# Optimization experiments

Hardware: AMD Instinct MI355X
Metric: run time of the kernel (lower is better)

The kernel has to match this reference:

```python
import jax, jax.numpy as jnp
import numpy as np

L = 6          # backbone GENConv layers
N = 100000     # nodes
E = 625000     # edges
F = 128        # gnn_in_features
HID = 64       # learner hidden width
NTOT = 200000  # node-feature table rows
TASKS = 112    # num_tasks
LN_EPS = 1e-5
MSG_EPS = 1e-7


def setup_inputs() -> dict:
    key = jax.random.key(0)
    ks = iter(jax.random.split(key, 40))

    def w(shape, fan):
        return jax.random.normal(next(ks), shape, jnp.float32) / np.float32(np.sqrt(fan))

    inp = {}
    inp["x"] = jax.random.uniform(next(ks), (N, 8), jnp.float32)
    inp["node_index"] = jax.random.randint(next(ks), (N,), 0, NTOT)
    inp["edge_index"] = jax.random.randint(next(ks), (2, E), 0, N)
    inp["edge_attr"] = jax.random.normal(next(ks), (E, 8), jnp.float32)
    inp["node_features_table"] = jax.random.normal(next(ks), (NTOT, 8), jnp.float32)
    inp["W_ohe"] = w((8, 8), 8); inp["b_ohe"] = jnp.zeros((8,), jnp.float32)
    inp["W_enc"] = w((16, F), 16); inp["b_enc"] = jnp.zeros((F,), jnp.float32)
    inp["W_edge"] = w((8, F), 8); inp["b_edge"] = jnp.zeros((F,), jnp.float32)
    inp["learner_W1"] = w((L + 1, F, HID), F); inp["learner_b1"] = jnp.zeros((L + 1, HID), jnp.float32)
    inp["learner_W2"] = w((L + 1, HID, F), HID); inp["learner_b2"] = jnp.zeros((L + 1, F), jnp.float32)
    inp["gcn_W"] = w((L, F, F), F); inp["gcn_b"] = jnp.zeros((L, F), jnp.float32)
    inp["gcn_t"] = jnp.ones((L,), jnp.float32)   # learnable softmax temperature
    inp["ln_gamma"] = jnp.ones((L, F), jnp.float32); inp["ln_beta"] = jnp.zeros((L, F), jnp.float32)
    inp["W_pred"] = w((F, TASKS), F); inp["b_pred"] = jnp.zeros((TASKS,), jnp.float32)
    return inp


def _layer_norm(h, g, b):
    mu = jnp.mean(h, -1, keepdims=True)
    var = jnp.mean(jnp.square(h - mu), -1, keepdims=True)
    return g * (h - mu) * jax.lax.rsqrt(var + LN_EPS) + b


def _learner(z, W1, b1, W2, b2):
    # NodeWeightLearner: 2-layer MLP with LeakyReLU(0.2), sigmoid gate per node/feature
    z = jax.nn.leaky_relu(z @ W1 + b1, 0.2)
    return jax.nn.sigmoid(z @ W2 + b2)


def reference(x, node_index, edge_index, edge_attr, node_features_table,
              W_ohe, b_ohe, W_enc, b_enc, W_edge, b_edge,
              learner_W1, learner_b1, learner_W2, learner_b2,
              gcn_W, gcn_b, gcn_t, ln_gamma, ln_beta, W_pred, b_pred):
    src, dst = edge_index[0], edge_index[1]
    n = x.shape[0]

    nf = jnp.concatenate([node_features_table[node_index], x @ W_ohe + b_ohe], axis=1)  # [N,16]
    h = nf @ W_enc + b_enc                                                              # [N,F]
    nw = _learner(h, learner_W1[0], learner_b1[0], learner_W2[0], learner_b2[0])
    h = h * nw
    codebank = h * nw
    edge_emb = edge_attr @ W_edge + b_edge                                              # [E,F]

    for l in range(L):
        # GENConv with softmax aggregation: m_e = relu(x_src + e) + eps, segment-softmax over dst
        m = jax.nn.relu(h[src] + edge_emb) + MSG_EPS          # [E,F]
        s = m * gcn_t[l]
        mx = jax.ops.segment_max(s, dst, num_segments=n)
        e = jnp.exp(s - mx[dst])
        denom = jax.ops.segment_sum(e, dst, num_segments=n)
        alpha = e / (denom[dst] + 1e-16)
        agg = jax.ops.segment_sum(alpha * m, dst, num_segments=n)  # [N,F]
        h1 = (h + agg) @ gcn_W[l] + gcn_b[l]                        # GENConv MLP (mlp_layers=1)
        h = jax.nn.relu(_layer_norm(h1, ln_gamma[l], ln_beta[l]))
        nw = _learner(h + codebank, learner_W1[l + 1], learner_b1[l + 1],
                      learner_W2[l + 1], learner_b2[l + 1])
        h_f = h * nw
        h = h_f + codebank * (1.0 - nw)    # highway combine
        codebank = codebank + h_f          # codebank update
        # dropout p=0.0 / eval mode -> identity

    return codebank @ W_pred + b_pred
```

## Files before the change

kernel.cpp:

```cpp
#include <hip/hip_runtime.h>
#include <stdint.h>

#define NN 100000
#define EE 625000
#define FF 128
#define HH 64
#define LL 6
#define TT 112

#define SCAN_CHUNK 2048
#define SCAN_NB ((NN + SCAN_CHUNK - 1) / SCAN_CHUNK)

typedef unsigned short u16;
typedef unsigned int u32;
typedef __attribute__((ext_vector_type(8))) short bf16x8;
typedef __attribute__((ext_vector_type(4))) float f32x4;

#define OFF_X    0u
#define OFF_TB   800000u
#define OFF_WO   2400000u
#define OFF_BO   2400064u
#define OFF_WE   2400072u
#define OFF_BE   2402120u
#define OFF_WED  2402248u
#define OFF_BED  2403272u
#define OFF_LW1  2403400u
#define OFF_LB1  2460744u
#define OFF_LW2  2461192u
#define OFF_LB2  2518536u
#define OFF_GW   2519432u
#define OFF_GB   2617736u
#define OFF_GT   2618504u
#define OFF_LG   2618512u
#define OFF_LB   2619280u
#define OFF_WP   2620048u
#define OFF_BP   2634384u
#define CANON_N  2634496u

__device__ __forceinline__ float bf2f(u16 u) { return __uint_as_float(((u32)u) << 16); }
__device__ __forceinline__ float bflo(u32 u) { return __uint_as_float(u << 16); }
__device__ __forceinline__ float bfhi(u32 u) { return __uint_as_float(u & 0xffff0000u); }
__device__ __forceinline__ u16 f2bf(float f) {
    u32 u = __float_as_uint(f);
    u32 r = u + 0x7fffu + ((u >> 16) & 1u);
    return (u16)(r >> 16);
}
__device__ __forceinline__ u32 pack2bf(float lo, float hi) {
    return ((u32)f2bf(hi) << 16) | (u32)f2bf(lo);
}
__device__ __forceinline__ uint4 pack8bf(const float* f) {
    uint4 r;
    r.x = pack2bf(f[0], f[1]); r.y = pack2bf(f[2], f[3]);
    r.z = pack2bf(f[4], f[5]); r.w = pack2bf(f[6], f[7]);
    return r;
}
__device__ __forceinline__ void unpack8bf(uint4 u, float* f) {
    f[0] = bflo(u.x); f[1] = bfhi(u.x); f[2] = bflo(u.y); f[3] = bfhi(u.y);
    f[4] = bflo(u.z); f[5] = bfhi(u.z); f[6] = bflo(u.w); f[7] = bfhi(u.w);
}
__device__ __forceinline__ bool is_f32(const u32* gt_raw) {
    return (gt_raw[0] & 0xFFFFu) == 0u;
}

template<bool CB32>
__device__ __forceinline__ float4 cb_ld(const void* cb, size_t row, int v) {
    if (CB32) {
        return ((const float4*)cb)[row * 32 + v];
    } else {
        uint2 u = ((const uint2*)cb)[row * 32 + v];
        float4 r; r.x = bflo(u.x); r.y = bfhi(u.x); r.z = bflo(u.y); r.w = bfhi(u.y);
        return r;
    }
}
template<bool CB32>
__device__ __forceinline__ void cb_st(void* cb, size_t row, int v, float4 val) {
    if (CB32) {
        ((float4*)cb)[row * 32 + v] = val;
    } else {
        uint2 u; u.x = pack2bf(val.x, val.y); u.y = pack2bf(val.z, val.w);
        ((uint2*)cb)[row * 32 + v] = u;
    }
}

struct ConvPtrs { const void* p[19]; };

__global__ __launch_bounds__(256) void k_convw(ConvPtrs ps, u16* __restrict__ wc) {
    u32 idx = blockIdx.x * 256 + threadIdx.x;
    if (idx >= CANON_N) return;
    const u32 offs[19] = {OFF_X, OFF_TB, OFF_WO, OFF_BO, OFF_WE, OFF_BE, OFF_WED, OFF_BED,
                          OFF_LW1, OFF_LB1, OFF_LW2, OFF_LB2, OFF_GW, OFF_GB, OFF_GT,
                          OFF_LG, OFF_LB, OFF_WP, OFF_BP};
    int seg = 0;
#pragma unroll
    for (int s = 1; s < 19; s++) if (idx >= offs[s]) seg = s;
    u32 e = idx - offs[seg];
    u16 v;
    if (seg == 14 && e >= 6u) {
        v = 0;
    } else {
        bool f32 = is_f32((const u32*)ps.p[14]);
        v = f32 ? f2bf(((const float*)ps.p[seg])[e]) : ((const u16*)ps.p[seg])[e];
    }
    wc[idx] = v;
}

__global__ __launch_bounds__(256) void k_twt(const u16* __restrict__ wc, u16* __restrict__ wt) {
    int idx = blockIdx.x * 256 + threadIdx.x;
    if (idx >= LL * FF * FF) return;
    int l = idx >> 14, r = (idx >> 7) & 127, c = idx & 127;
    wt[idx] = wc[OFF_GW + l * FF * FF + c * FF + r];
}

__global__ __launch_bounds__(256) void k_twl(const u16* __restrict__ wc,
                                             u16* __restrict__ w1t, u16* __restrict__ w2t,
                                             u16* __restrict__ wet) {
    int idx = blockIdx.x * 256 + threadIdx.x;
    const int HALF = 7 * FF * HH;
    if (idx < HALF) {
        int ls = idx / (FF * HH), rem = idx % (FF * HH);
        int n = rem / FF, k = rem % FF;
        w1t[idx] = wc[OFF_LW1 + ls * FF * HH + k * HH + n];
    } else if (idx < 2 * HALF) {
        int j = idx - HALF;
        int ls = j / (FF * HH), rem = j % (FF * HH);
        int n = rem / HH, k = rem % HH;
        w2t[j] = wc[OFF_LW2 + ls * FF * HH + k * FF + n];
    } else if (idx < 2 * HALF + FF * 32) {
        int j = idx - 2 * HALF;
        int n = j >> 5, k = j & 31;
        wet[j] = (k < 16) ? wc[OFF_WE + k * FF + n] : (u16)0;
    }
}

__global__ void k_hist(const int* __restrict__ dst, int* __restrict__ counts) {
    int e = blockIdx.x * 256 + threadIdx.x;
    if (e < EE) atomicAdd(&counts[dst[e]], 1);
}

__global__ void k_scan1(const int* __restrict__ counts, int* __restrict__ bsums) {
    __shared__ int red[256];
    int t = threadIdx.x;
    int base = blockIdx.x * SCAN_CHUNK + t * 8;
    int s = 0;
#pragma unroll
    for (int j = 0; j < 8; j++) { int i = base + j; s += (i < NN) ? counts[i] : 0; }
    red[t] = s; __syncthreads();
    for (int off = 128; off > 0; off >>= 1) {
        if (t < off) red[t] += red[t + off];
        __syncthreads();
    }
    if (t == 0) bsums[blockIdx.x] = red[0];
}

__global__ void k_scan2(int* __restrict__ bsums, int* __restrict__ row_ptr) {
    __shared__ int v[256];
    int t = threadIdx.x;
    int x = (t < SCAN_NB) ? bsums[t] : 0;
    v[t] = x; __syncthreads();
    for (int off = 1; off < 256; off <<= 1) {
        int add = (t >= off) ? v[t - off] : 0;
        __syncthreads();
        v[t] += add;
        __syncthreads();
    }
    if (t < SCAN_NB) bsums[t] = v[t] - x;
    if (t == 0) row_ptr[NN] = EE;
}

__global__ void k_scan3(int* counts_cursor, int* __restrict__ row_ptr,
                        const int* __restrict__ bsums) {
    __shared__ int red[256];
    int t = threadIdx.x;
    int base = blockIdx.x * SCAN_CHUNK + t * 8;
    int c[8]; int s = 0;
#pragma unroll
    for (int j = 0; j < 8; j++) { int i = base + j; c[j] = (i < NN) ? counts_cursor[i] : 0; s += c[j]; }
    red[t] = s; __syncthreads();
    int own = s;
    for (int off = 1; off < 256; off <<= 1) {
        int add = (t >= off) ? red[t - off] : 0;
        __syncthreads();
        red[t] += add;
        __syncthreads();
    }
    int off0 = bsums[blockIdx.x] + red[t] - own;
    int run = 0;
#pragma unroll
    for (int j = 0; j < 8; j++) {
        int i = base + j;
        if (i < NN) { row_ptr[i] = off0 + run; counts_cursor[i] = off0 + run; }
        run += c[j];
    }
}

__global__ void k_scatter(const int* __restrict__ src, const int* __restrict__ dst,
                          const void* __restrict__ edge_attr, const u32* __restrict__ gt_raw,
                          int* __restrict__ cursor, int* __restrict__ s_src,
                          u16* __restrict__ s_attr) {
    int e = blockIdx.x * 256 + threadIdx.x;
    if (e >= EE) return;
    int d = dst[e];
    int p = atomicAdd(&cursor[d], 1);
    s_src[p] = src[e];
    if (is_f32(gt_raw)) {
        const float4* ea = (const float4*)edge_attr;
        float4 lo = ea[(size_t)e * 2], hi = ea[(size_t)e * 2 + 1];
        float f[8] = {lo.x, lo.y, lo.z, lo.w, hi.x, hi.y, hi.z, hi.w};
        ((uint4*)s_attr)[p] = pack8bf(f);
    } else {
        ((uint4*)s_attr)[p] = ((const uint4*)edge_attr)[e];
    }
}

template<bool CB32>
__global__ __launch_bounds__(256) void k_encoder(const u16* __restrict__ wc,
                                                 const int* __restrict__ node_index,
                                                 const u16* __restrict__ wet,
                                                 const u16* __restrict__ w1t,
                                                 const u16* __restrict__ w2t,
                                                 u16* __restrict__ h_out, void* cb_out) {
    __shared__ float sOutF[4][16 * 132];
    __shared__ alignas(16) u16 sH[4][16 * 136];
    __shared__ alignas(16) u16 sZh[4][16 * 72];
    __shared__ alignas(16) u16 sZl[4][16 * 72];
    __shared__ float sWo[64], sbo[8];
    int t = threadIdx.x;
    if (t < 64) sWo[t] = bf2f(wc[OFF_WO + t]);
    if (t < 8) sbo[t] = bf2f(wc[OFF_BO + t]);
    __syncthreads();

    int wave = t >> 6, lane = t & 63;
    int quad = lane >> 4, l15 = lane & 15;
    int base = blockIdx.x * 64 + wave * 16;
    int nodeA = base + l15; if (nodeA >= NN) nodeA = NN - 1;

    uint4 afu = make_uint4(0u, 0u, 0u, 0u);
    if (quad == 0) {
        afu = ((const uint4*)(wc + OFF_TB))[node_index[nodeA]];
    } else if (quad == 1) {
        uint4 xv4 = ((const uint4*)(wc + OFF_X))[nodeA];
        float xv[8]; unpack8bf(xv4, xv);
        float o[8];
#pragma unroll
        for (int j = 0; j < 8; j++) {
            float a = sbo[j];
#pragma unroll
            for (int i = 0; i < 8; i++) a += xv[i] * sWo[i * 8 + j];
            o[j] = a;
        }
        afu = pack8bf(o);
    }
    bf16x8 af = __builtin_bit_cast(bf16x8, afu);

    f32x4 acch[8];
#pragma unroll
    for (int nt = 0; nt < 8; nt++) {
        float bv = bf2f(wc[OFF_BE + nt * 16 + l15]);
        f32x4 v; v[0] = bv; v[1] = bv; v[2] = bv; v[3] = bv;
        acch[nt] = v;
    }
#pragma unroll
    for (int nt = 0; nt < 8; nt++) {
        uint4 wb = ((const uint4*)(wet + (size_t)(nt * 16 + l15) * 32))[quad];
        bf16x8 bfrag = __builtin_bit_cast(bf16x8, wb);
        acch[nt] = __builtin_amdgcn_mfma_f32_16x16x32_bf16(af, bfrag, acch[nt], 0, 0, 0);
    }
    u16* hw = sH[wave];
#pragma unroll
    for (int nt = 0; nt < 8; nt++)
#pragma unroll
        for (int r = 0; r < 4; r++)
            hw[(quad * 4 + r) * 136 + nt * 16 + l15] = f2bf(acch[nt][r]);

    f32x4 acc1[4];
#pragma unroll
    for (int nt = 0; nt < 4; nt++) {
        float bv = bf2f(wc[OFF_LB1 + nt * 16 + l15]);
        f32x4 v; v[0] = bv; v[1] = bv; v[2] = bv; v[3] = bv;
        acc1[nt] = v;
    }
#pragma unroll
    for (int kc = 0; kc < 4; kc++) {
        bf16x8 a1 = __builtin_bit_cast(bf16x8,
                        *(const uint4*)(hw + l15 * 136 + kc * 32 + quad * 8));
#pragma unroll
        for (int nt = 0; nt < 4; nt++) {
            uint4 wb = ((const uint4*)(w1t + (size_t)(nt * 16 + l15) * FF))[kc * 4 + quad];
            bf16x8 bfrag = __builtin_bit_cast(bf16x8, wb);
            acc1[nt] = __builtin_amdgcn_mfma_f32_16x16x32_bf16(a1, bfrag, acc1[nt], 0, 0, 0);
        }
    }
    u16* zh = sZh[wave];
    u16* zl = sZl[wave];
#pragma unroll
    for (int nt = 0; nt < 4; nt++)
#pragma unroll
        for (int r = 0; r < 4; r++) {
            float v = acc1[nt][r];
            v = fmaxf(v, 0.2f * v);
            u16 hi16 = f2bf(v);
            float resid = v - bf2f(hi16);
            zh[(quad * 4 + r) * 72 + nt * 16 + l15] = hi16;
            zl[(quad * 4 + r) * 72 + nt * 16 + l15] = f2bf(resid);
        }
    bf16x8 a2h[2], a2l[2];
#pragma unroll
    for (int kc2 = 0; kc2 < 2; kc2++) {
        a2h[kc2] = __builtin_bit_cast(bf16x8,
                       *(const uint4*)(zh + l15 * 72 + kc2 * 32 + quad * 8));
        a2l[kc2] = __builtin_bit_cast(bf16x8,
                       *(const uint4*)(zl + l15 * 72 + kc2 * 32 + quad * 8));
    }
    f32x4 acc2[8];
#pragma unroll
    for (int nt = 0; nt < 8; nt++) {
        float bv = bf2f(wc[OFF_LB2 + nt * 16 + l15]);
        f32x4 v; v[0] = bv; v[1] = bv; v[2] = bv; v[3] = bv;
        acc2[nt] = v;
    }
#pragma unroll
    for (int kc2 = 0; kc2 < 2; kc2++)
#pragma unroll
        for (int nt = 0; nt < 8; nt++) {
            uint4 wb = ((const uint4*)(w2t + (size_t)(nt * 16 + l15) * HH))[kc2 * 4 + quad];
            bf16x8 bfrag = __builtin_bit_cast(bf16x8, wb);
            acc2[nt] = __builtin_amdgcn_mfma_f32_16x16x32_bf16(a2h[kc2], bfrag, acc2[nt], 0, 0, 0);
            acc2[nt] = __builtin_amdgcn_mfma_f32_16x16x32_bf16(a2l[kc2], bfrag, acc2[nt], 0, 0, 0);
        }
    float* myf = sOutF[wave];
#pragma unroll
    for (int nt = 0; nt < 8; nt++)
#pragma unroll
        for (int r = 0; r < 4; r++)
            myf[(quad * 4 + r) * 132 + nt * 16 + l15] = acc2[nt][r];
    int orow = lane >> 2, ocol = lane & 3;
    int onode = base + orow;
    if (onode < NN) {
        uint4* ho4 = (uint4*)(h_out + (size_t)onode * FF);
#pragma unroll
        for (int u = 0; u < 4; u++) {
            int k0 = ocol * 32 + u * 8;
            float f[8];
            unpack8bf(*(const uint4*)(hw + orow * 136 + k0), f);
            float4 lg1 = *(const float4*)(myf + orow * 132 + k0);
            float4 lg2 = *(const float4*)(myf + orow * 132 + k0 + 4);
            float lg[8] = {lg1.x, lg1.y, lg1.z, lg1.w, lg2.x, lg2.y, lg2.z, lg2.w};
            float ho[8], co[8];
#pragma unroll
            for (int j = 0; j < 8; j++) {
                float nw = 1.f / (1.f + __expf(-lg[j]));
                float hwv = f[j] * nw;
                ho[j] = hwv; co[j] = hwv * nw;
            }
            ho4[ocol * 4 + u] = pack8bf(ho);
            cb_st<CB32>(cb_out, (size_t)onode, k0 / 4, make_float4(co[0], co[1], co[2], co[3]));
            cb_st<CB32>(cb_out, (size_t)onode, k0 / 4 + 1, make_float4(co[4], co[5], co[6], co[7]));
        }
    }
}

__global__ __launch_bounds__(256) void k_agg(const u16* __restrict__ h,
                                             const int* __restrict__ row_ptr,
                                             const int* __restrict__ s_src,
                                             const u16* __restrict__ s_attr,
                                             const u16* __restrict__ wc, int layer,
                                             u16* __restrict__ agg) {
    int t = threadIdx.x;
    int hw = t >> 5, lane = t & 31;
    int node = blockIdx.x * 8 + hw;
    if (node >= NN) return;
    uint2 wcol[8];
#pragma unroll
    for (int k = 0; k < 8; k++) wcol[k] = ((const uint2*)(wc + OFF_WED))[k * 32 + lane];
    uint2 bcol = ((const uint2*)(wc + OFF_BED))[lane];
    float b0 = bflo(bcol.x), b1 = bfhi(bcol.x), b2 = bflo(bcol.y), b3 = bfhi(bcol.y);
    float tl = bf2f(wc[OFF_GT + layer]);
    int beg = row_ptr[node], end = row_ptr[node + 1];
    float n0 = 0.f, n1 = 0.f, n2 = 0.f, n3 = 0.f;
    float d0 = 0.f, d1 = 0.f, d2 = 0.f, d3 = 0.f;
    for (int i = beg; i < end; i++) {
        int sid = s_src[i];
        uint2 hv = ((const uint2*)h)[(size_t)sid * 32 + lane];
        uint4 av = ((const uint4*)s_attr)[i];
        float a[8]; unpack8bf(av, a);
        float e0 = b0, e1 = b1, e2 = b2, e3 = b3;
#pragma unroll
        for (int k = 0; k < 8; k++) {
            e0 += a[k] * bflo(wcol[k].x); e1 += a[k] * bfhi(wcol[k].x);
            e2 += a[k] * bflo(wcol[k].y); e3 += a[k] * bfhi(wcol[k].y);
        }
        float m0 = fmaxf(bflo(hv.x) + e0, 0.f) + 1e-7f;
        float m1 = fmaxf(bfhi(hv.x) + e1, 0.f) + 1e-7f;
        float m2 = fmaxf(bflo(hv.y) + e2, 0.f) + 1e-7f;
        float m3 = fmaxf(bfhi(hv.y) + e3, 0.f) + 1e-7f;
        float x0 = __expf(tl * m0), x1 = __expf(tl * m1);
        float x2 = __expf(tl * m2), x3 = __expf(tl * m3);
        n0 += x0 * m0; n1 += x1 * m1; n2 += x2 * m2; n3 += x3 * m3;
        d0 += x0; d1 += x1; d2 += x2; d3 += x3;
    }
    uint2 r;
    r.x = pack2bf(n0 / (d0 + 1e-16f), n1 / (d1 + 1e-16f));
    r.y = pack2bf(n2 / (d2 + 1e-16f), n3 / (d3 + 1e-16f));
    ((uint2*)agg)[(size_t)node * 32 + lane] = r;
}

#define OSTR 136
__global__ __launch_bounds__(256) void k_gcn(const u16* __restrict__ h,
                                             u16* hb,
                                             const u16* __restrict__ wc,
                                             const u16* __restrict__ wt, int layer) {
    __shared__ alignas(16) u16 sOut[4][16 * OSTR];
    int t = threadIdx.x;
    int wave = t >> 6, lane = t & 63;
    int quad = lane >> 4, l15 = lane & 15;
    int base = blockIdx.x * 64 + wave * 16;
    int nodeA = base + l15; if (nodeA >= NN) nodeA = NN - 1;
    const u16* wtl = wt + (size_t)layer * FF * FF;

    f32x4 acc[8];
#pragma unroll
    for (int nt = 0; nt < 8; nt++) {
        float bv = bf2f(wc[OFF_GB + layer * FF + nt * 16 + l15]);
        f32x4 v; v[0] = bv; v[1] = bv; v[2] = bv; v[3] = bv;
        acc[nt] = v;
    }
#pragma unroll
    for (int kc = 0; kc < 4; kc++) {
        uint4 ha = ((const uint4*)(h + (size_t)nodeA * FF))[kc * 4 + quad];
        uint4 aa = ((const uint4*)(hb + (size_t)nodeA * FF))[kc * 4 + quad];
        float hf[8], af[8], sm[8];
        unpack8bf(ha, hf); unpack8bf(aa, af);
#pragma unroll
        for (int j = 0; j < 8; j++) sm[j] = hf[j] + af[j];
        uint4 pa = pack8bf(sm);
        bf16x8 afrag = __builtin_bit_cast(bf16x8, pa);
#pragma unroll
        for (int nt = 0; nt < 8; nt++) {
            uint4 wb = ((const uint4*)(wtl + (size_t)(nt * 16 + l15) * FF))[kc * 4 + quad];
            bf16x8 bfrag = __builtin_bit_cast(bf16x8, wb);
            acc[nt] = __builtin_amdgcn_mfma_f32_16x16x32_bf16(afrag, bfrag, acc[nt], 0, 0, 0);
        }
    }
    u16* my = sOut[wave];
#pragma unroll
    for (int nt = 0; nt < 8; nt++)
#pragma unroll
        for (int r = 0; r < 4; r++)
            my[(quad * 4 + r) * OSTR + nt * 16 + l15] = f2bf(acc[nt][r]);
    int orow = lane >> 2, ocol = lane & 3;
    int onode = base + orow;
    if (onode < NN) {
        uint4* dst = (uint4*)(hb + (size_t)onode * FF);
        const uint4* srcl = (const uint4*)(my + orow * OSTR);
#pragma unroll
        for (int u = 0; u < 4; u++) dst[ocol * 4 + u] = srcl[ocol * 4 + u];
    }
}

template<bool CB32>
__global__ __launch_bounds__(256) void k_post(const u16* __restrict__ h1,
                                              void* cbv,
                                              u16* __restrict__ h_out,
                                              const u16* __restrict__ wc,
                                              const u16* __restrict__ w1t,
                                              const u16* __restrict__ w2t, int layer) {
    __shared__ float sOutF[4][16 * 132];
    __shared__ alignas(16) u16 zt[4][16 * 72];
    __shared__ float smu[4][16], srstd[4][16];
    __shared__ float sg[FF], sbt[FF], sb1[HH], sb2[FF];
    int t = threadIdx.x;
    int ls = layer + 1;
    if (t < FF) {
        sg[t] = bf2f(wc[OFF_LG + layer * FF + t]);
        sbt[t] = bf2f(wc[OFF_LB + layer * FF + t]);
        sb2[t] = bf2f(wc[OFF_LB2 + ls * FF + t]);
    }
    if (t < HH) sb1[t] = bf2f(wc[OFF_LB1 + ls * HH + t]);
    __syncthreads();

    int wave = t >> 6, lane = t & 63;
    int quad = lane >> 4, l15 = lane & 15;
    int base = blockIdx.x * 64 + wave * 16;
    int nodeA = base + l15; if (nodeA >= NN) nodeA = NN - 1;
    const u16* w1l = w1t + (size_t)ls * HH * FF;
    const u16* w2l = w2t + (size_t)ls * FF * HH;

    const uint4* h4 = (const uint4*)(h1 + (size_t)nodeA * FF);
    uint4 hreg[4];
    float s = 0.f, s2 = 0.f;
#pragma unroll
    for (int kc = 0; kc < 4; kc++) {
        hreg[kc] = h4[kc * 4 + quad];
        float f[8]; unpack8bf(hreg[kc], f);
#pragma unroll
        for (int j = 0; j < 8; j++) { s += f[j]; s2 += f[j] * f[j]; }
    }
    s += __shfl_xor(s, 16); s += __shfl_xor(s, 32);
    s2 += __shfl_xor(s2, 16); s2 += __shfl_xor(s2, 32);
    float mu = s * (1.f / 128.f);
    float var = fmaxf(s2 * (1.f / 128.f) - mu * mu, 0.f);
    float rstd = rsqrtf(var + 1e-5f);
    if (quad == 0) { smu[wave][l15] = mu; srstd[wave][l15] = rstd; }

    f32x4 acc1[4];
#pragma unroll
    for (int nt = 0; nt < 4; nt++) {
        float bv = sb1[nt * 16 + l15];
        f32x4 v; v[0] = bv; v[1] = bv; v[2] = bv; v[3] = bv;
        acc1[nt] = v;
    }
#pragma unroll
    for (int kc = 0; kc < 4; kc++) {
        float f[8]; unpack8bf(hreg[kc], f);
        int k0 = kc * 32 + quad * 8;
        float4 ca = cb_ld<CB32>(cbv, (size_t)nodeA, kc * 8 + quad * 2);
        float4 cq = cb_ld<CB32>(cbv, (size_t)nodeA, kc * 8 + quad * 2 + 1);
        float cv[8] = {ca.x, ca.y, ca.z, ca.w, cq.x, cq.y, cq.z, cq.w};
        float sv[8];
#pragma unroll
        for (int j = 0; j < 8; j++) {
            float hl = fmaxf(sg[k0 + j] * (f[j] - mu) * rstd + sbt[k0 + j], 0.f);
            sv[j] = hl + cv[j];
        }
        uint4 ahi = pack8bf(sv);
        float thi[8]; unpack8bf(ahi, thi);
        float rv[8];
#pragma unroll
        for (int j = 0; j < 8; j++) rv[j] = sv[j] - thi[j];
        uint4 alo = pack8bf(rv);
        bf16x8 fhi = __builtin_bit_cast(bf16x8, ahi);
        bf16x8 flo = __builtin_bit_cast(bf16x8, alo);
#pragma unroll
        for (int nt = 0; nt < 4; nt++) {
            uint4 wb = ((const uint4*)(w1l + (size_t)(nt * 16 + l15) * FF))[kc * 4 + quad];
            bf16x8 bfrag = __builtin_bit_cast(bf16x8, wb);
            acc1[nt] = __builtin_amdgcn_mfma_f32_16x16x32_bf16(fhi, bfrag, acc1[nt], 0, 0, 0);
            acc1[nt] = __builtin_amdgcn_mfma_f32_16x16x32_bf16(flo, bfrag, acc1[nt], 0, 0, 0);
        }
    }
    u16* ztw = zt[wave];
#pragma unroll
    for (int nt = 0; nt < 4; nt++)
#pragma unroll
        for (int r = 0; r < 4; r++) {
            float v = acc1[nt][r];
            v = fmaxf(v, 0.2f * v);
            ztw[(quad * 4 + r) * 72 + nt * 16 + l15] = f2bf(v);
        }
    bf16x8 a2[2];
#pragma unroll
    for (int kc2 = 0; kc2 < 2; kc2++)
        a2[kc2] = __builtin_bit_cast(bf16x8,
                      *(const uint4*)(ztw + l15 * 72 + kc2 * 32 + quad * 8));
    f32x4 acc2[8];
#pragma unroll
    for (int nt = 0; nt < 8; nt++) {
        float bv = sb2[nt * 16 + l15];
        f32x4 v; v[0] = bv; v[1] = bv; v[2] = bv; v[3] = bv;
        acc2[nt] = v;
    }
#pragma unroll
    for (int kc2 = 0; kc2 < 2; kc2++)
#pragma unroll
        for (int nt = 0; nt < 8; nt++) {
            uint4 wb = ((const uint4*)(w2l + (size_t)(nt * 16 + l15) * HH))[kc2 * 4 + quad];
            bf16x8 bfrag = __builtin_bit_cast(bf16x8, wb);
            acc2[nt] = __builtin_amdgcn_mfma_f32_16x16x32_bf16(a2[kc2], bfrag, acc2[nt], 0, 0, 0);
        }
    float* myf = sOutF[wave];
#pragma unroll
    for (int nt = 0; nt < 8; nt++)
#pragma unroll
        for (int r = 0; r < 4; r++)
            myf[(quad * 4 + r) * 132 + nt * 16 + l15] = acc2[nt][r];
    int orow = lane >> 2, ocol = lane & 3;
    int onode = base + orow;
    if (onode < NN) {
        float mu2 = smu[wave][orow], rstd2 = srstd[wave][orow];
        const uint4* h4n = (const uint4*)(h1 + (size_t)onode * FF);
        uint4* ho4 = (uint4*)(h_out + (size_t)onode * FF);
#pragma unroll
        for (int u = 0; u < 4; u++) {
            int k0 = ocol * 32 + u * 8;
            float f[8]; unpack8bf(h4n[ocol * 4 + u], f);
            float4 lg1 = *(const float4*)(myf + orow * 132 + k0);
            float4 lg2 = *(const float4*)(myf + orow * 132 + k0 + 4);
            float lg[8] = {lg1.x, lg1.y, lg1.z, lg1.w, lg2.x, lg2.y, lg2.z, lg2.w};
            float4 ca = cb_ld<CB32>(cbv, (size_t)onode, k0 / 4);
            float4 cq = cb_ld<CB32>(cbv, (size_t)onode, k0 / 4 + 1);
            float cv[8] = {ca.x, ca.y, ca.z, ca.w, cq.x, cq.y, cq.z, cq.w};
            float ho[8], co[8];
#pragma unroll
            for (int j = 0; j < 8; j++) {
                float hl = fmaxf(sg[k0 + j] * (f[j] - mu2) * rstd2 + sbt[k0 + j], 0.f);
                float nw = 1.f / (1.f + __expf(-lg[j]));
                float hf = hl * nw;
                ho[j] = hf + cv[j] * (1.f - nw);
                co[j] = cv[j] + hf;
            }
            ho4[ocol * 4 + u] = pack8bf(ho);
            cb_st<CB32>(cbv, (size_t)onode, k0 / 4, make_float4(co[0], co[1], co[2], co[3]));
            cb_st<CB32>(cbv, (size_t)onode, k0 / 4 + 1, make_float4(co[4], co[5], co[6], co[7]));
        }
    }
}

template<bool CB32>
__global__ __launch_bounds__(256) void k_pred(const void* __restrict__ cbv,
                                              const u16* __restrict__ wc,
                                              const u32* __restrict__ gt_raw,
                                              void* __restrict__ outv) {
    __shared__ alignas(16) u16 sW[FF * TT];
    __shared__ float sb[TT];
    int t = threadIdx.x;
    { const uint4* s4 = (const uint4*)(wc + OFF_WP); uint4* d4 = (uint4*)sW;
      for (int i = t; i < 1792; i += 256) d4[i] = s4[i]; }
    if (t < TT) sb[t] = bf2f(wc[OFF_BP + t]);
    __syncthreads();
    int n = blockIdx.x * 256 + t;
    if (n >= NN) return;
    bool f32o = is_f32(gt_raw);
    const uint2* w2 = (const uint2*)sW;
    for (int c = 0; c < 4; c++) {
        float acc[28];
#pragma unroll
        for (int j = 0; j < 28; j++) acc[j] = sb[c * 28 + j];
        for (int k4 = 0; k4 < 32; k4++) {
            float4 hv = cb_ld<CB32>(cbv, n, k4);
            float ha[4] = {hv.x, hv.y, hv.z, hv.w};
#pragma unroll
            for (int kq = 0; kq < 4; kq++) {
                int k = k4 * 4 + kq;
                float hk = ha[kq];
#pragma unroll
                for (int q = 0; q < 7; q++) {
                    uint2 w = w2[28 * k + 7 * c + q];
                    acc[q * 4 + 0] += hk * bflo(w.x); acc[q * 4 + 1] += hk * bfhi(w.x);
                    acc[q * 4 + 2] += hk * bflo(w.y); acc[q * 4 + 3] += hk * bfhi(w.y);
                }
            }
        }
        if (f32o) {
            float4* o4 = (float4*)((float*)outv + (size_t)n * TT + c * 28);
#pragma unroll
            for (int q = 0; q < 7; q++)
                o4[q] = make_float4(acc[q * 4], acc[q * 4 + 1], acc[q * 4 + 2], acc[q * 4 + 3]);
        } else {
            uint2* o2 = (uint2*)((u16*)outv + (size_t)n * TT + c * 28);
#pragma unroll
            for (int q = 0; q < 7; q++) {
                uint2 r;
                r.x = pack2bf(acc[q * 4 + 0], acc[q * 4 + 1]);
                r.y = pack2bf(acc[q * 4 + 2], acc[q * 4 + 3]);
                o2[q] = r;
            }
        }
    }
}

extern "C" void kernel_launch(void* const* d_in, const int* in_sizes, int n_in,
                              void* d_out, int out_size, void* d_ws, size_t ws_size,
                              hipStream_t stream) {
    const int* node_index = (const int*)d_in[1];
    const int* edge_index = (const int*)d_in[2];
    const u32* gt_raw = (const u32*)d_in[17];

    ConvPtrs ps;
    ps.p[0] = d_in[0];
    ps.p[1] = d_in[4];
    ps.p[2] = d_in[5];  ps.p[3] = d_in[6];
    ps.p[4] = d_in[7];  ps.p[5] = d_in[8];
    ps.p[6] = d_in[9];  ps.p[7] = d_in[10];
    ps.p[8] = d_in[11]; ps.p[9] = d_in[12];
    ps.p[10] = d_in[13]; ps.p[11] = d_in[14];
    ps.p[12] = d_in[15]; ps.p[13] = d_in[16];
    ps.p[14] = d_in[17];
    ps.p[15] = d_in[18]; ps.p[16] = d_in[19];
    ps.p[17] = d_in[20]; ps.p[18] = d_in[21];

    auto pad = [](size_t b) { return (b + 255) & ~(size_t)255; };
    const size_t B_h = pad((size_t)NN * FF * 2);
    const size_t B_h1 = pad((size_t)(NN + 1) * FF * 2);
    const size_t B_cb32 = pad((size_t)(NN + 1) * FF * 4);
    const size_t B_cb16 = pad((size_t)(NN + 1) * FF * 2);
    const size_t B_attr = pad((size_t)EE * 8 * 2);
    const size_t B_src = pad((size_t)EE * 4);
    const size_t B_rp = pad((size_t)(NN + 1) * 4);
    const size_t B_cur = pad((size_t)NN * 4);
    const size_t B_bs = pad(256 * 4);
    const size_t B_wc = pad((size_t)CANON_N * 2);
    const size_t B_wt = pad((size_t)LL * FF * FF * 2);
    const size_t B_wlt = pad((size_t)7 * FF * HH * 2);
    const size_t B_wet = pad((size_t)FF * 32 * 2);
    size_t fixed = B_h1 + B_h + B_attr + B_src + B_rp + B_cur + B_bs + B_wc + B_wt
                 + 2 * B_wlt + B_wet;
    bool cb32 = (fixed + B_cb32) <= ws_size;

    char* w = (char*)d_ws;
    size_t off = 0;
    auto alloc = [&](size_t bytes) -> void* { void* p = w + off; off += bytes; return p; };
    u16* h_a = (u16*)alloc(B_h1);
    u16* hb = (u16*)alloc(B_h);
    void* cb = alloc(cb32 ? B_cb32 : B_cb16);
    u16* s_attr = (u16*)alloc(B_attr);
    int* s_src = (int*)alloc(B_src);
    int* row_ptr = (int*)alloc(B_rp);
    int* cursor = (int*)alloc(B_cur);
    int* bsums = (int*)alloc(B_bs);
    u16* wc = (u16*)alloc(B_wc);
    u16* wt = (u16*)alloc(B_wt);
    u16* w1t = (u16*)alloc(B_wlt);
    u16* w2t = (u16*)alloc(B_wlt);
    u16* wet = (u16*)alloc(B_wet);

    const int GE = (EE + 255) / 256;
    const int GN = (NN + 255) / 256;
    const int GA = (NN + 7) / 8;
    const int GC = (CANON_N + 255) / 256;
    const int GG = (NN + 63) / 64;
    const int GT6 = (LL * FF * FF + 255) / 256;
    const int GTL = (2 * 7 * FF * HH + FF * 32 + 255) / 256;

    hipMemsetAsync(cursor, 0, (size_t)NN * 4, stream);
    k_convw<<<GC, 256, 0, stream>>>(ps, wc);
    k_twt<<<GT6, 256, 0, stream>>>(wc, wt);
    k_twl<<<GTL, 256, 0, stream>>>(wc, w1t, w2t, wet);
    k_hist<<<GE, 256, 0, stream>>>(edge_index + EE, cursor);
    k_scan1<<<SCAN_NB, 256, 0, stream>>>(cursor, bsums);
    k_scan2<<<1, 256, 0, stream>>>(bsums, row_ptr);
    k_scan3<<<SCAN_NB, 256, 0, stream>>>(cursor, row_ptr, bsums);
    k_scatter<<<GE, 256, 0, stream>>>(edge_index, edge_index + EE, d_in[3], gt_raw,
                                      cursor, s_src, s_attr);

    if (cb32) k_encoder<true><<<GG, 256, 0, stream>>>(wc, node_index, wet, w1t, w2t, h_a, cb);
    else      k_encoder<false><<<GG, 256, 0, stream>>>(wc, node_index, wet, w1t, w2t, h_a, cb);

    for (int l = 0; l < LL; l++) {
        k_agg<<<GA, 256, 0, stream>>>(h_a, row_ptr, s_src, s_attr, wc, l, hb);
        k_gcn<<<GG, 256, 0, stream>>>(h_a, hb, wc, wt, l);
        if (cb32) k_post<true><<<GG, 256, 0, stream>>>(hb, cb, h_a, wc, w1t, w2t, l);
        else      k_post<false><<<GG, 256, 0, stream>>>(hb, cb, h_a, wc, w1t, w2t, l);
    }
    if (cb32) k_pred<true><<<GN, 256, 0, stream>>>(cb, wc, gt_raw, d_out);
    else      k_pred<false><<<GN, 256, 0, stream>>>(cb, wc, gt_raw, d_out);
}
```

Before: 1.514 ms.

## Fuse GENConv GEMM into post kernel and move prediction head to MFMA

Merges the per-layer GCN linear kernel into the layernorm/learner post kernel, so the GEMM output h1 stays in shared memory rather than round-tripping through global memory, and one launch per layer is dropped. The final prediction head is rewritten from a scalar FMA loop over an LDS-staged weight to bf16 MFMA, using a pre-transposed weight. When the codebank is kept in fp32, a hi/lo bf16 split preserves precision. Shared-memory use per block in the fused kernel grows, which may reduce occupancy.

```diff
diff --git a/kernel.cpp b/kernel.cpp
--- a/kernel.cpp
+++ b/kernel.cpp
@@ -113,9 +113,10 @@
 
 __global__ __launch_bounds__(256) void k_twl(const u16* __restrict__ wc,
                                              u16* __restrict__ w1t, u16* __restrict__ w2t,
-                                             u16* __restrict__ wet) {
+                                             u16* __restrict__ wet, u16* __restrict__ wpt) {
     int idx = blockIdx.x * 256 + threadIdx.x;
     const int HALF = 7 * FF * HH;
+    const int WETN = FF * 32;
     if (idx < HALF) {
         int ls = idx / (FF * HH), rem = idx % (FF * HH);
         int n = rem / FF, k = rem % FF;
@@ -125,10 +126,14 @@
         int ls = j / (FF * HH), rem = j % (FF * HH);
         int n = rem / HH, k = rem % HH;
         w2t[j] = wc[OFF_LW2 + ls * FF * HH + k * FF + n];
-    } else if (idx < 2 * HALF + FF * 32) {
+    } else if (idx < 2 * HALF + WETN) {
         int j = idx - 2 * HALF;
         int n = j >> 5, k = j & 31;
         wet[j] = (k < 16) ? wc[OFF_WE + k * FF + n] : (u16)0;
+    } else if (idx < 2 * HALF + WETN + TT * FF) {
+        int j = idx - 2 * HALF - WETN;
+        int n = j >> 7, k = j & 127;
+        wpt[j] = wc[OFF_WP + k * TT + n];
     }
 }
 
@@ -404,66 +409,15 @@
     ((uint2*)agg)[(size_t)node * 32 + lane] = r;
 }
 
-#define OSTR 136
-__global__ __launch_bounds__(256) void k_gcn(const u16* __restrict__ h,
-                                             u16* hb,
-                                             const u16* __restrict__ wc,
-                                             const u16* __restrict__ wt, int layer) {
-    __shared__ alignas(16) u16 sOut[4][16 * OSTR];
-    int t = threadIdx.x;
-    int wave = t >> 6, lane = t & 63;
-    int quad = lane >> 4, l15 = lane & 15;
-    int base = blockIdx.x * 64 + wave * 16;
-    int nodeA = base + l15; if (nodeA >= NN) nodeA = NN - 1;
-    const u16* wtl = wt + (size_t)layer * FF * FF;
-
-    f32x4 acc[8];
-#pragma unroll
-    for (int nt = 0; nt < 8; nt++) {
-        float bv = bf2f(wc[OFF_GB + layer * FF + nt * 16 + l15]);
-        f32x4 v; v[0] = bv; v[1] = bv; v[2] = bv; v[3] = bv;
-        acc[nt] = v;
-    }
-#pragma unroll
-    for (int kc = 0; kc < 4; kc++) {
-        uint4 ha = ((const uint4*)(h + (size_t)nodeA * FF))[kc * 4 + quad];
-        uint4 aa = ((const uint4*)(hb + (size_t)nodeA * FF))[kc * 4 + quad];
-        float hf[8], af[8], sm[8];
-        unpack8bf(ha, hf); unpack8bf(aa, af);
-#pragma unroll
-        for (int j = 0; j < 8; j++) sm[j] = hf[j] + af[j];
-        uint4 pa = pack8bf(sm);
-        bf16x8 afrag = __builtin_bit_cast(bf16x8, pa);
-#pragma unroll
-        for (int nt = 0; nt < 8; nt++) {
-            uint4 wb = ((const uint4*)(wtl + (size_t)(nt * 16 + l15) * FF))[kc * 4 + quad];
-            bf16x8 bfrag = __builtin_bit_cast(bf16x8, wb);
-            acc[nt] = __builtin_amdgcn_mfma_f32_16x16x32_bf16(afrag, bfrag, acc[nt], 0, 0, 0);
-        }
-    }
-    u16* my = sOut[wave];
-#pragma unroll
-    for (int nt = 0; nt < 8; nt++)
-#pragma unroll
-        for (int r = 0; r < 4; r++)
-            my[(quad * 4 + r) * OSTR + nt * 16 + l15] = f2bf(acc[nt][r]);
-    int orow = lane >> 2, ocol = lane & 3;
-    int onode = base + orow;
-    if (onode < NN) {
-        uint4* dst = (uint4*)(hb + (size_t)onode * FF);
-        const uint4* srcl = (const uint4*)(my + orow * OSTR);
-#pragma unroll
-        for (int u = 0; u < 4; u++) dst[ocol * 4 + u] = srcl[ocol * 4 + u];
-    }
-}
-
 template<bool CB32>
-__global__ __launch_bounds__(256) void k_post(const u16* __restrict__ h1,
-                                              void* cbv,
-                                              u16* __restrict__ h_out,
-                                              const u16* __restrict__ wc,
-                                              const u16* __restrict__ w1t,
-                                              const u16* __restrict__ w2t, int layer) {
+__global__ __launch_bounds__(256) void k_gcnpost(const u16* __restrict__ hb,
+                                                 u16* ha,
+                                                 void* cbv,
+                                                 const u16* __restrict__ wc,
+                                                 const u16* __restrict__ wt,
+                                                 const u16* __restrict__ w1t,
+                                                 const u16* __restrict__ w2t, int layer) {
+    __shared__ alignas(16) u16 sH1[4][16 * 136];
     __shared__ float sOutF[4][16 * 132];
     __shared__ alignas(16) u16 zt[4][16 * 72];
     __shared__ float smu[4][16], srstd[4][16];
@@ -482,15 +436,46 @@
     int quad = lane >> 4, l15 = lane & 15;
     int base = blockIdx.x * 64 + wave * 16;
     int nodeA = base + l15; if (nodeA >= NN) nodeA = NN - 1;
+    const u16* wtl = wt + (size_t)layer * FF * FF;
     const u16* w1l = w1t + (size_t)ls * HH * FF;
     const u16* w2l = w2t + (size_t)ls * FF * HH;
 
-    const uint4* h4 = (const uint4*)(h1 + (size_t)nodeA * FF);
+    f32x4 accg[8];
+#pragma unroll
+    for (int nt = 0; nt < 8; nt++) {
+        float bv = bf2f(wc[OFF_GB + layer * FF + nt * 16 + l15]);
+        f32x4 v; v[0] = bv; v[1] = bv; v[2] = bv; v[3] = bv;
+        accg[nt] = v;
+    }
+#pragma unroll
+    for (int kc = 0; kc < 4; kc++) {
+        uint4 hv = ((const uint4*)(ha + (size_t)nodeA * FF))[kc * 4 + quad];
+        uint4 aa = ((const uint4*)(hb + (size_t)nodeA * FF))[kc * 4 + quad];
+        float hf[8], af[8], sm[8];
+        unpack8bf(hv, hf); unpack8bf(aa, af);
+#pragma unroll
+        for (int j = 0; j < 8; j++) sm[j] = hf[j] + af[j];
+        uint4 pa = pack8bf(sm);
+        bf16x8 afrag = __builtin_bit_cast(bf16x8, pa);
+#pragma unroll
+        for (int nt = 0; nt < 8; nt++) {
+            uint4 wb = ((const uint4*)(wtl + (size_t)(nt * 16 + l15) * FF))[kc * 4 + quad];
+            bf16x8 bfrag = __builtin_bit_cast(bf16x8, wb);
+            accg[nt] = __builtin_amdgcn_mfma_f32_16x16x32_bf16(afrag, bfrag, accg[nt], 0, 0, 0);
+        }
+    }
+    u16* hw = sH1[wave];
+#pragma unroll
+    for (int nt = 0; nt < 8; nt++)
+#pragma unroll
+        for (int r = 0; r < 4; r++)
+            hw[(quad * 4 + r) * 136 + nt * 16 + l15] = f2bf(accg[nt][r]);
+
     uint4 hreg[4];
     float s = 0.f, s2 = 0.f;
 #pragma unroll
     for (int kc = 0; kc < 4; kc++) {
-        hreg[kc] = h4[kc * 4 + quad];
+        hreg[kc] = *(const uint4*)(hw + l15 * 136 + kc * 32 + quad * 8);
         float f[8]; unpack8bf(hreg[kc], f);
 #pragma unroll
         for (int j = 0; j < 8; j++) { s += f[j]; s2 += f[j] * f[j]; }
@@ -577,12 +562,12 @@
     int onode = base + orow;
     if (onode < NN) {
         float mu2 = smu[wave][orow], rstd2 = srstd[wave][orow];
-        const uint4* h4n = (const uint4*)(h1 + (size_t)onode * FF);
-        uint4* ho4 = (uint4*)(h_out + (size_t)onode * FF);
+        uint4* ho4 = (uint4*)(ha + (size_t)onode * FF);
 #pragma unroll
         for (int u = 0; u < 4; u++) {
             int k0 = ocol * 32 + u * 8;
-            float f[8]; unpack8bf(h4n[ocol * 4 + u], f);
+            float f[8];
+            unpack8bf(*(const uint4*)(hw + orow * 136 + k0), f);
             float4 lg1 = *(const float4*)(myf + orow * 132 + k0);
             float4 lg2 = *(const float4*)(myf + orow * 132 + k0 + 4);
             float lg[8] = {lg1.x, lg1.y, lg1.z, lg1.w, lg2.x, lg2.y, lg2.z, lg2.w};
@@ -608,50 +593,68 @@
 template<bool CB32>
 __global__ __launch_bounds__(256) void k_pred(const void* __restrict__ cbv,
                                               const u16* __restrict__ wc,
+                                              const u16* __restrict__ wpt,
                                               const u32* __restrict__ gt_raw,
                                               void* __restrict__ outv) {
-    __shared__ alignas(16) u16 sW[FF * TT];
-    __shared__ float sb[TT];
+    __shared__ float sOutF[4][16 * 116];
     int t = threadIdx.x;
-    { const uint4* s4 = (const uint4*)(wc + OFF_WP); uint4* d4 = (uint4*)sW;
-      for (int i = t; i < 1792; i += 256) d4[i] = s4[i]; }
-    if (t < TT) sb[t] = bf2f(wc[OFF_BP + t]);
-    __syncthreads();
-    int n = blockIdx.x * 256 + t;
-    if (n >= NN) return;
+    int wave = t >> 6, lane = t & 63;
+    int quad = lane >> 4, l15 = lane & 15;
+    int base = blockIdx.x * 64 + wave * 16;
+    int nodeA = base + l15; if (nodeA >= NN) nodeA = NN - 1;
     bool f32o = is_f32(gt_raw);
-    const uint2* w2 = (const uint2*)sW;
-    for (int c = 0; c < 4; c++) {
-        float acc[28];
-#pragma unroll
-        for (int j = 0; j < 28; j++) acc[j] = sb[c * 28 + j];
-        for (int k4 = 0; k4 < 32; k4++) {
-            float4 hv = cb_ld<CB32>(cbv, n, k4);
-            float ha[4] = {hv.x, hv.y, hv.z, hv.w};
-#pragma unroll
-            for (int kq = 0; kq < 4; kq++) {
-                int k = k4 * 4 + kq;
-                float hk = ha[kq];
-#pragma unroll
-                for (int q = 0; q < 7; q++) {
-                    uint2 w = w2[28 * k + 7 * c + q];
-                    acc[q * 4 + 0] += hk * bflo(w.x); acc[q * 4 + 1] += hk * bfhi(w.x);
-                    acc[q * 4 + 2] += hk * bflo(w.y); acc[q * 4 + 3] += hk * bfhi(w.y);
-                }
-            }
-        }
+
+    f32x4 acc[7];
+#pragma unroll
+    for (int nt = 0; nt < 7; nt++) {
+        float bv = bf2f(wc[OFF_BP + nt * 16 + l15]);
+        f32x4 v; v[0] = bv; v[1] = bv; v[2] = bv; v[3] = bv;
+        acc[nt] = v;
+    }
+#pragma unroll
+    for (int kc = 0; kc < 4; kc++) {
+        float4 ca = cb_ld<CB32>(cbv, (size_t)nodeA, kc * 8 + quad * 2);
+        float4 cq = cb_ld<CB32>(cbv, (size_t)nodeA, kc * 8 + quad * 2 + 1);
+        float cv[8] = {ca.x, ca.y, ca.z, ca.w, cq.x, cq.y, cq.z, cq.w};
+        uint4 ahi = pack8bf(cv);
+        bf16x8 fhi = __builtin_bit_cast(bf16x8, ahi);
+        bf16x8 flo;
+        if (CB32) {
+            float thi[8]; unpack8bf(ahi, thi);
+            float rv[8];
+#pragma unroll
+            for (int j = 0; j < 8; j++) rv[j] = cv[j] - thi[j];
+            flo = __builtin_bit_cast(bf16x8, pack8bf(rv));
+        }
+#pragma unroll
+        for (int nt = 0; nt < 7; nt++) {
+            uint4 wb = ((const uint4*)(wpt + (size_t)(nt * 16 + l15) * FF))[kc * 4 + quad];
+            bf16x8 bfrag = __builtin_bit_cast(bf16x8, wb);
+            acc[nt] = __builtin_amdgcn_mfma_f32_16x16x32_bf16(fhi, bfrag, acc[nt], 0, 0, 0);
+            if (CB32)
+                acc[nt] = __builtin_amdgcn_mfma_f32_16x16x32_bf16(flo, bfrag, acc[nt], 0, 0, 0);
+        }
+    }
+    float* myf = sOutF[wave];
+#pragma unroll
+    for (int nt = 0; nt < 7; nt++)
+#pragma unroll
+        for (int r = 0; r < 4; r++)
+            myf[(quad * 4 + r) * 116 + nt * 16 + l15] = acc[nt][r];
+    int orow = lane >> 2, ocol = lane & 3;
+    int onode = base + orow;
+    if (onode < NN) {
         if (f32o) {
-            float4* o4 = (float4*)((float*)outv + (size_t)n * TT + c * 28);
+            float4* o4 = (float4*)((float*)outv + (size_t)onode * TT + ocol * 28);
 #pragma unroll
             for (int q = 0; q < 7; q++)
-                o4[q] = make_float4(acc[q * 4], acc[q * 4 + 1], acc[q * 4 + 2], acc[q * 4 + 3]);
+                o4[q] = *(const float4*)(myf + orow * 116 + ocol * 28 + q * 4);
         } else {
-            uint2* o2 = (uint2*)((u16*)outv + (size_t)n * TT + c * 28);
+            uint2* o2 = (uint2*)((u16*)outv + (size_t)onode * TT + ocol * 28);
 #pragma unroll
             for (int q = 0; q < 7; q++) {
-                uint2 r;
-                r.x = pack2bf(acc[q * 4 + 0], acc[q * 4 + 1]);
-                r.y = pack2bf(acc[q * 4 + 2], acc[q * 4 + 3]);
+                const float* p = myf + orow * 116 + ocol * 28 + q * 4;
+                uint2 r; r.x = pack2bf(p[0], p[1]); r.y = pack2bf(p[2], p[3]);
                 o2[q] = r;
             }
         }
@@ -692,8 +695,9 @@
     const size_t B_wt = pad((size_t)LL * FF * FF * 2);
     const size_t B_wlt = pad((size_t)7 * FF * HH * 2);
     const size_t B_wet = pad((size_t)FF * 32 * 2);
+    const size_t B_wpt = pad((size_t)TT * FF * 2);
     size_t fixed = B_h1 + B_h + B_attr + B_src + B_rp + B_cur + B_bs + B_wc + B_wt
-                 + 2 * B_wlt + B_wet;
+                 + 2 * B_wlt + B_wet + B_wpt;
     bool cb32 = (fixed + B_cb32) <= ws_size;
 
     char* w = (char*)d_ws;
@@ -712,19 +716,19 @@
     u16* w1t = (u16*)alloc(B_wlt);
     u16* w2t = (u16*)alloc(B_wlt);
     u16* wet = (u16*)alloc(B_wet);
+    u16* wpt = (u16*)alloc(B_wpt);
 
     const int GE = (EE + 255) / 256;
-    const int GN = (NN + 255) / 256;
     const int GA = (NN + 7) / 8;
     const int GC = (CANON_N + 255) / 256;
     const int GG = (NN + 63) / 64;
     const int GT6 = (LL * FF * FF + 255) / 256;
-    const int GTL = (2 * 7 * FF * HH + FF * 32 + 255) / 256;
+    const int GTL = (2 * 7 * FF * HH + FF * 32 + TT * FF + 255) / 256;
 
     hipMemsetAsync(cursor, 0, (size_t)NN * 4, stream);
     k_convw<<<GC, 256, 0, stream>>>(ps, wc);
     k_twt<<<GT6, 256, 0, stream>>>(wc, wt);
-    k_twl<<<GTL, 256, 0, stream>>>(wc, w1t, w2t, wet);
+    k_twl<<<GTL, 256, 0, stream>>>(wc, w1t, w2t, wet, wpt);
     k_hist<<<GE, 256, 0, stream>>>(edge_index + EE, cursor);
     k_scan1<<<SCAN_NB, 256, 0, stream>>>(cursor, bsums);
     k_scan2<<<1, 256, 0, stream>>>(bsums, row_ptr);
@@ -737,10 +741,9 @@
 
     for (int l = 0; l < LL; l++) {
         k_agg<<<GA, 256, 0, stream>>>(h_a, row_ptr, s_src, s_attr, wc, l, hb);
-        k_gcn<<<GG, 256, 0, stream>>>(h_a, hb, wc, wt, l);
-        if (cb32) k_post<true><<<GG, 256, 0, stream>>>(hb, cb, h_a, wc, w1t, w2t, l);
-        else      k_post<false><<<GG, 256, 0, stream>>>(hb, cb, h_a, wc, w1t, w2t, l);
-    }
-    if (cb32) k_pred<true><<<GN, 256, 0, stream>>>(cb, wc, gt_raw, d_out);
-    else      k_pred<false><<<GN, 256, 0, stream>>>(cb, wc, gt_raw, d_out);
-}
+        if (cb32) k_gcnpost<true><<<GG, 256, 0, stream>>>(hb, h_a, cb, wc, wt, w1t, w2t, l);
+        else      k_gcnpost<false><<<GG, 256, 0, stream>>>(hb, h_a, cb, wc, wt, w1t, w2t, l);
+    }
+    if (cb32) k_pred<true><<<GG, 256, 0, stream>>>(cb, wc, wpt, gt_raw, d_out);
+    else      k_pred<false><<<GG, 256, 0, stream>>>(cb, wc, wpt, gt_raw, d_out);
+}
```

Measured after the change: 1.347 ms. 1.12x faster.
